# Kernel optimization log

Hardware: AMD Instinct MI355X
Metric: run time of the kernel (lower is better)

The kernel has to match this reference:

```python
import jax, jax.numpy as jnp
import numpy as np
from jax import lax

INPUT_DIM = 1024
HIDDEN_DIM = 2048
N, L = 64, 512


def setup_inputs() -> dict:
    key = jax.random.key(0)
    ks = jax.random.split(key, 6)
    X = jax.random.normal(ks[0], (N, L, INPUT_DIM), dtype=jnp.float32)
    H0 = jnp.zeros((N, HIDDEN_DIM), dtype=jnp.float32)
    # G-invariant layer params (DeepSets invariant map): out = w * sum(x) + b, one per gate (i,f,g,o)
    inv_scale = 1.0 / np.sqrt(INPUT_DIM)
    inv_w = jax.random.normal(ks[1], (4, HIDDEN_DIM), dtype=jnp.float32) * inv_scale
    inv_b = jax.random.normal(ks[2], (4, HIDDEN_DIM), dtype=jnp.float32) * inv_scale
    # Linear(hidden, hidden) per gate, torch convention W: (out, in)
    lin_scale = 1.0 / np.sqrt(HIDDEN_DIM)
    lin_W = jax.random.normal(ks[3], (4, HIDDEN_DIM, HIDDEN_DIM), dtype=jnp.float32) * lin_scale
    lin_b = jax.random.normal(ks[4], (4, HIDDEN_DIM), dtype=jnp.float32) * lin_scale
    return {"X": X, "H0": H0, "inv_w": inv_w, "inv_b": inv_b, "lin_W": lin_W, "lin_b": lin_b}


def reference(X, H0, inv_w, inv_b, lin_W, lin_b):
    # X: (N, L, D); H0: (N, H)
    def step(carry, x_t):
        h, c = carry                               # (N, H), (N, H)
        s = jnp.sum(x_t, axis=-1, keepdims=True)   # (N, 1) invariant statistic
        inv = s * inv_w[:, None, :] + inv_b[:, None, :]            # (4, N, H)
        lin = jnp.einsum('nh,gkh->gnk', h, lin_W) + lin_b[:, None, :]  # (4, N, H)
        z = inv + lin
        i = jax.nn.sigmoid(z[0])
        f = jax.nn.sigmoid(z[1])
        g = jnp.tanh(z[2])
        o = jax.nn.sigmoid(z[3])
        c = f * c + i * g
        h = o * jnp.tanh(c)
        return (h, c), None

    Xt = jnp.swapaxes(X, 0, 1)                     # (L, N, D)
    (h, _), _ = lax.scan(step, (H0, jnp.zeros_like(H0)), Xt)
    # original returns swapdims(hidden_state, 0, 1) -> (H, N)
    return h.T
```

## Files before the change

kernel.cpp:

```cpp
#include <hip/hip_runtime.h>
#include <hip/hip_fp16.h>


typedef _Float16 f16x8 __attribute__((ext_vector_type(8)));
typedef float    f32x4 __attribute__((ext_vector_type(4)));
typedef unsigned long long u64;

static __device__ __forceinline__ float fast_sig(float x) {
  return 1.f / (1.f + __expf(-x));
}
static __device__ __forceinline__ float fast_tanh(float x) {
  x = fminf(15.f, fmaxf(-15.f, x));
  const float e = __expf(2.f * x);
  return (e - 1.f) / (e + 1.f);
}

static __device__ __forceinline__ void st_h16(void* p, float v) {
  const unsigned short b = __builtin_bit_cast(unsigned short, (_Float16)v);
  __hip_atomic_store((unsigned short*)p, b, __ATOMIC_RELAXED, __HIP_MEMORY_SCOPE_AGENT);
}
static __device__ __forceinline__ void st_h64(void* p, u64 v) {
  __hip_atomic_store((u64*)p, v, __ATOMIC_RELAXED, __HIP_MEMORY_SCOPE_AGENT);
}

static __device__ __forceinline__ int h_off(int n, int j) {
  return ((n >> 4) << 16) + ((j >> 5) << 10) + ((n & 15) << 6) +
         (((j >> 3) & 3) << 4) + ((j & 7) << 1);
}

__global__ void __launch_bounds__(256) seq_sum_kernel(const float* __restrict__ X,
                                                      float* s_all) {
  const int gw   = (int)((blockIdx.x * blockDim.x + threadIdx.x) >> 6);
  const int lane = threadIdx.x & 63;
  const int n = gw >> 9, t = gw & 511;
  const float4* p = (const float4*)(X + ((size_t)gw << 10));
  float s = 0.f;
#pragma unroll
  for (int i = 0; i < 4; ++i) {
    const float4 v = p[lane + (i << 6)];
    s += (v.x + v.y) + (v.z + v.w);
  }
#pragma unroll
  for (int off = 32; off; off >>= 1) s += __shfl_xor(s, off);
  if (lane == 0) s_all[(t << 6) + n] = s;
}

__global__ void bar_init_kernel(unsigned* bar) {
  bar[threadIdx.x]       = 0u;
  bar[threadIdx.x + 256] = 0u;
  bar[threadIdx.x + 512] = 0u;
  bar[threadIdx.x + 768] = 0u;
}

static __device__ __forceinline__ void grid_barrier2(unsigned* bar, unsigned round,
                                                     int tid, int blk) {
  asm volatile("s_waitcnt vmcnt(0)" ::: "memory");
  __syncthreads();
  if (tid == 0) {
    unsigned* grp  = bar + ((blk & 7) << 5);
    unsigned* root = bar + 512;
    const unsigned old =
        __hip_atomic_fetch_add(grp, 1u, __ATOMIC_RELAXED, __HIP_MEMORY_SCOPE_AGENT);
    if (old == 32u * round - 1u)
      __hip_atomic_fetch_add(root, 1u, __ATOMIC_RELAXED, __HIP_MEMORY_SCOPE_AGENT);
    const unsigned target = 8u * round;
    unsigned guard = 0;
    while (__hip_atomic_load(root, __ATOMIC_RELAXED, __HIP_MEMORY_SCOPE_AGENT) <
           target) {
      __builtin_amdgcn_s_sleep(1);
      if (++guard > (1u << 23)) break;
    }
  }
  __syncthreads();
}

#define LOAD4(d0, d1, d2, d3, addr)                                         \
  asm volatile("global_load_dwordx4 %0, %4, off sc1\n\t"                    \
               "global_load_dwordx4 %1, %4, off offset:1024 sc1\n\t"        \
               "global_load_dwordx4 %2, %4, off offset:2048 sc1\n\t"        \
               "global_load_dwordx4 %3, %4, off offset:3072 sc1"            \
               : "=&v"(d0), "=&v"(d1), "=&v"(d2), "=&v"(d3)                 \
               : "v"(addr)                                                  \
               : "memory")

#define WAITG(n, A)                                                         \
  asm volatile("s_waitcnt vmcnt(" #n ")"                                    \
               : "+v"(A[0]), "+v"(A[1]), "+v"(A[2]), "+v"(A[3]),            \
                 "+v"(A[4]), "+v"(A[5]), "+v"(A[6]), "+v"(A[7]),            \
                 "+v"(A[8]), "+v"(A[9]), "+v"(A[10]), "+v"(A[11]),          \
                 "+v"(A[12]), "+v"(A[13]), "+v"(A[14]), "+v"(A[15])         \
               :                                                            \
               : "memory")

#define KMATH(A)                                                            \
  _Pragma("unroll")                                                         \
  for (int i_ = 0; i_ < 16; ++i_) {                                         \
    acc[0] = __builtin_amdgcn_mfma_f32_16x16x32_f16(A[i_], Wr[i_][0],       \
                                                    acc[0], 0, 0, 0);       \
    acc[1] = __builtin_amdgcn_mfma_f32_16x16x32_f16(A[i_], Wr[i_][1],       \
                                                    acc[1], 0, 0, 0);       \
    acc[2] = __builtin_amdgcn_mfma_f32_16x16x32_f16(A[i_], Wr[i_][2],       \
                                                    acc[2], 0, 0, 0);       \
    acc[3] = __builtin_amdgcn_mfma_f32_16x16x32_f16(A[i_], Wr[i_][3],       \
                                                    acc[3], 0, 0, 0);       \
  }

#define SCATTER(bt)                                                         \
  _Pragma("unroll")                                                         \
  for (int ct_ = 0; ct_ < 4; ++ct_) {                                       \
    const int kf_ = ct_ * 4 + (cc >> 2);                                    \
    _Pragma("unroll")                                                       \
    for (int v_ = 0; v_ < 4; ++v_) {                                        \
      const int n_  = (bt) * 16 + (q << 2) + v_;                            \
      const int key = (n_ & 15) ^ (n_ >> 4);                                \
      red[wave][n_][((kf_ ^ key) << 2) + (cc & 3)] = acc[ct_][v_];          \
    }                                                                       \
  }

__global__ void __launch_bounds__(256, 1) ginv_lstm_persist(
    const float* __restrict__ lin_W, const float* __restrict__ inv_w,
    const float* __restrict__ inv_b, const float* __restrict__ lin_b,
    const float* s_all, const float* __restrict__ H0,
    _Float16* hb0, _Float16* hb1, unsigned* bar, float* out) {
  __shared__ __align__(16) float red[12][32][64];
  __shared__ __align__(16) _Float16 hx[32][16];
  const int blk = blockIdx.x;
  const int tid = threadIdx.x;
  _Float16* hbuf[2] = {hb0, hb1};

  const int fblk = blk & 127;
  const int nh   = blk >> 7;

  const int wave = tid >> 6;
  const int lane = tid & 63;
  const int q    = lane >> 4;
  const int cc   = lane & 15;

  f16x8 Wr[16][4];
#pragma unroll
  for (int ct = 0; ct < 4; ++ct) {
    const int kf = ct * 4 + (cc >> 2), g = cc & 3;
    const float* wrow =
        lin_W + (((size_t)(g * 2048 + fblk * 16 + kf)) << 11) + wave * 512 + q * 8;
#pragma unroll
    for (int kc = 0; kc < 16; ++kc) {
      const float4 va = *(const float4*)(wrow + kc * 32);
      const float4 vb = *(const float4*)(wrow + kc * 32 + 4);
      f16x8 f;
      f[0] = (_Float16)va.x; f[1] = (_Float16)va.y;
      f[2] = (_Float16)va.z; f[3] = (_Float16)va.w;
      f[4] = (_Float16)vb.x; f[5] = (_Float16)vb.y;
      f[6] = (_Float16)vb.z; f[7] = (_Float16)vb.w;
      Wr[kc][ct] = f;
    }
  }

  {
    int i0 = blk * 512 + tid;
    st_h16((char*)hb0 + h_off(i0 >> 11, i0 & 2047), H0[i0]);
    i0 += 256;
    st_h16((char*)hb0 + h_off(i0 >> 11, i0 & 2047), H0[i0]);
  }

  const int nloc = lane & 31;
  const int nb   = lane >> 5;
  float iw[2][4], ibb[2][4];
#pragma unroll
  for (int kk = 0; kk < 2; ++kk) {
    const int kf = wave + (nb << 2) + (kk << 3);
    const int Kg = fblk * 16 + kf;
#pragma unroll
    for (int g = 0; g < 4; ++g) {
      iw[kk][g]  = inv_w[(g << 11) + Kg];
      ibb[kk][g] = inv_b[(g << 11) + Kg] + lin_b[(g << 11) + Kg];
    }
  }

  unsigned round = 1;
  grid_barrier2(bar, round, tid, blk);

  float cst[2] = {0.f, 0.f};

  const int ld_base = ((nh * 2) << 16) + (wave << 14) + (cc << 6) + (q << 4);
  const int st_off = ((nh * 2 + (tid >> 4)) << 16) + ((fblk >> 1) << 10) +
                     ((tid & 15) << 6) + ((fblk & 1) << 5);

  for (int t = 0; t < 512; ++t) {
    const char* hpb = (const char*)hbuf[t & 1] + ld_base;

    const float sv = s_all[(t << 6) + nh * 32 + nloc];

    f16x8 pa[16], pb[16];
    f32x4 acc[4];

#pragma unroll
    for (int w = 0; w < 4; ++w)
      LOAD4(pa[w * 4], pa[w * 4 + 1], pa[w * 4 + 2], pa[w * 4 + 3],
            hpb + (w << 12));
#pragma unroll
    for (int w = 0; w < 4; ++w)
      LOAD4(pb[w * 4], pb[w * 4 + 1], pb[w * 4 + 2], pb[w * 4 + 3],
            hpb + 65536 + (w << 12));

    WAITG(16, pa);
#pragma unroll
    for (int ct = 0; ct < 4; ++ct) acc[ct] = (f32x4){0.f, 0.f, 0.f, 0.f};
    KMATH(pa);
    SCATTER(0);

    WAITG(0, pb);
#pragma unroll
    for (int ct = 0; ct < 4; ++ct) acc[ct] = (f32x4){0.f, 0.f, 0.f, 0.f};
    KMATH(pb);
    SCATTER(1);

    __syncthreads();

    float hnew[2];
    const int key = (nloc & 15) ^ (nloc >> 4);
#pragma unroll
    for (int kk = 0; kk < 2; ++kk) {
      const int kf  = wave + (nb << 2) + (kk << 3);
      const int off = (kf ^ key) << 2;
      f32x4 zz = *(const f32x4*)&red[0][nloc][off];
#pragma unroll
      for (int w = 1; w < 4; ++w) zz += *(const f32x4*)&red[w][nloc][off];
      const float zi = zz[0] + sv * iw[kk][0] + ibb[kk][0];
      const float zf = zz[1] + sv * iw[kk][1] + ibb[kk][1];
      const float zg = zz[2] + sv * iw[kk][2] + ibb[kk][2];
      const float zo = zz[3] + sv * iw[kk][3] + ibb[kk][3];
      const float ig = fast_sig(zi);
      const float fg = fast_sig(zf);
      const float gg = fast_tanh(zg);
      const float og = fast_sig(zo);
      const float cn = fg * cst[kk] + ig * gg;
      cst[kk] = cn;
      hnew[kk] = og * fast_tanh(cn);
    }

#pragma unroll
    for (int kk = 0; kk < 2; ++kk)
      hx[nloc][wave + (nb << 2) + (kk << 3)] = (_Float16)hnew[kk];
    __syncthreads();
    if (t < 511 && tid < 32) {
      union { f16x8 v; u64 w[2]; } u0, u1;
      u0.v = *(const f16x8*)&hx[tid][0];
      u1.v = *(const f16x8*)&hx[tid][8];
      char* dst = (char*)hbuf[(t + 1) & 1] + st_off;
      st_h64(dst,      u0.w[0]);
      st_h64(dst + 8,  u0.w[1]);
      st_h64(dst + 16, u1.w[0]);
      st_h64(dst + 24, u1.w[1]);
    }
    ++round;
    grid_barrier2(bar, round, tid, blk);
  }

  if (tid < 32) {
#pragma unroll
    for (int f = 0; f < 16; ++f)
      out[((fblk * 16 + f) << 6) + nh * 32 + tid] = (float)hx[tid][f];
  }
}

extern "C" void kernel_launch(void* const* d_in, const int* in_sizes, int n_in,
                              void* d_out, int out_size, void* d_ws, size_t ws_size,
                              hipStream_t stream) {
  const float* X     = (const float*)d_in[0];
  const float* H0    = (const float*)d_in[1];
  const float* inv_w = (const float*)d_in[2];
  const float* inv_b = (const float*)d_in[3];
  const float* lin_W = (const float*)d_in[4];
  const float* lin_b = (const float*)d_in[5];
  float* out = (float*)d_out;

  const size_t S_BYTES = 512 * 64 * 4;
  const size_t BAR_PAD = 4096;
  const size_t H_BYTES = 64 * 2048 * 2;
  const size_t NEED = S_BYTES + BAR_PAD + 2 * H_BYTES;

  float*    s_all;
  unsigned* bar;
  _Float16* hb[2];
  if (ws_size >= NEED) {
    char* ws = (char*)d_ws;
    s_all = (float*)ws;
    bar   = (unsigned*)(ws + S_BYTES);
    for (int i = 0; i < 2; ++i)
      hb[i] = (_Float16*)(ws + S_BYTES + BAR_PAD + (size_t)i * H_BYTES);
  } else {
    s_all = (float*)d_out;
    char* xt = (char*)d_in[0] + (size_t)64 * 512 * 1024 * 4 -
               (BAR_PAD + 2 * H_BYTES);
    bar = (unsigned*)xt;
    for (int i = 0; i < 2; ++i)
      hb[i] = (_Float16*)(xt + BAR_PAD + (size_t)i * H_BYTES);
  }

  seq_sum_kernel<<<8192, 256, 0, stream>>>(X, s_all);
  bar_init_kernel<<<1, 256, 0, stream>>>(bar);
  ginv_lstm_persist<<<256, 256, 0, stream>>>(lin_W, inv_w, inv_b, lin_b, s_all, H0,
                                             hb[0], hb[1], bar, out);
}
```

Before: 4.079 ms.

## Flatten grid barrier, store h directly per thread, preload sequence sums into LDS

```diff
diff --git a/kernel.cpp b/kernel.cpp
--- a/kernel.cpp
+++ b/kernel.cpp
@@ -19,8 +19,8 @@
   const unsigned short b = __builtin_bit_cast(unsigned short, (_Float16)v);
   __hip_atomic_store((unsigned short*)p, b, __ATOMIC_RELAXED, __HIP_MEMORY_SCOPE_AGENT);
 }
-static __device__ __forceinline__ void st_h64(void* p, u64 v) {
-  __hip_atomic_store((u64*)p, v, __ATOMIC_RELAXED, __HIP_MEMORY_SCOPE_AGENT);
+static __device__ __forceinline__ void st_h32(void* p, unsigned v) {
+  __hip_atomic_store((unsigned*)p, v, __ATOMIC_RELAXED, __HIP_MEMORY_SCOPE_AGENT);
 }
 
 static __device__ __forceinline__ int h_off(int n, int j) {
@@ -52,21 +52,22 @@
   bar[threadIdx.x + 768] = 0u;
 }
 
-static __device__ __forceinline__ void grid_barrier2(unsigned* bar, unsigned round,
-                                                     int tid, int blk) {
+static __device__ __forceinline__ void grid_barrier(unsigned* bar, unsigned round,
+                                                    int tid, int blk) {
   asm volatile("s_waitcnt vmcnt(0)" ::: "memory");
   __syncthreads();
   if (tid == 0) {
-    unsigned* grp  = bar + ((blk & 7) << 5);
-    unsigned* root = bar + 512;
-    const unsigned old =
-        __hip_atomic_fetch_add(grp, 1u, __ATOMIC_RELAXED, __HIP_MEMORY_SCOPE_AGENT);
-    if (old == 32u * round - 1u)
-      __hip_atomic_fetch_add(root, 1u, __ATOMIC_RELAXED, __HIP_MEMORY_SCOPE_AGENT);
-    const unsigned target = 8u * round;
+    __hip_atomic_fetch_add(bar + ((blk & 7) << 4), 1u, __ATOMIC_RELAXED,
+                           __HIP_MEMORY_SCOPE_AGENT);
+    const unsigned target = round << 8;
     unsigned guard = 0;
-    while (__hip_atomic_load(root, __ATOMIC_RELAXED, __HIP_MEMORY_SCOPE_AGENT) <
-           target) {
+    for (;;) {
+      unsigned s = 0;
+#pragma unroll
+      for (int i = 0; i < 8; ++i)
+        s += __hip_atomic_load(bar + (i << 4), __ATOMIC_RELAXED,
+                               __HIP_MEMORY_SCOPE_AGENT);
+      if (s >= target) break;
       __builtin_amdgcn_s_sleep(1);
       if (++guard > (1u << 23)) break;
     }
@@ -122,8 +123,8 @@
     const float* __restrict__ inv_b, const float* __restrict__ lin_b,
     const float* s_all, const float* __restrict__ H0,
     _Float16* hb0, _Float16* hb1, unsigned* bar, float* out) {
-  __shared__ __align__(16) float red[12][32][64];
-  __shared__ __align__(16) _Float16 hx[32][16];
+  __shared__ __align__(16) float s_lds[512][32];
+  __shared__ __align__(16) float red[4][32][64];
   const int blk = blockIdx.x;
   const int tid = threadIdx.x;
   _Float16* hbuf[2] = {hb0, hb1};
@@ -162,13 +163,18 @@
     st_h16((char*)hb0 + h_off(i0 >> 11, i0 & 2047), H0[i0]);
   }
 
-  const int nloc = lane & 31;
-  const int nb   = lane >> 5;
+  for (int i = tid; i < 512 * 8; i += 256) {
+    const int t4 = i >> 3, nl4 = (i & 7) << 2;
+    *(float4*)&s_lds[t4][nl4] =
+        *(const float4*)&s_all[(t4 << 6) + (nh << 5) + nl4];
+  }
+
+  const int nloc = (wave << 3) + (lane >> 3);
+  const int c0   = (lane & 7) << 1;
   float iw[2][4], ibb[2][4];
 #pragma unroll
   for (int kk = 0; kk < 2; ++kk) {
-    const int kf = wave + (nb << 2) + (kk << 3);
-    const int Kg = fblk * 16 + kf;
+    const int Kg = fblk * 16 + c0 + kk;
 #pragma unroll
     for (int g = 0; g < 4; ++g) {
       iw[kk][g]  = inv_w[(g << 11) + Kg];
@@ -177,18 +183,18 @@
   }
 
   unsigned round = 1;
-  grid_barrier2(bar, round, tid, blk);
+  grid_barrier(bar, round, tid, blk);
 
   float cst[2] = {0.f, 0.f};
+  float hnew[2] = {0.f, 0.f};
 
   const int ld_base = ((nh * 2) << 16) + (wave << 14) + (cc << 6) + (q << 4);
-  const int st_off = ((nh * 2 + (tid >> 4)) << 16) + ((fblk >> 1) << 10) +
-                     ((tid & 15) << 6) + ((fblk & 1) << 5);
+  const int hst_off = ((nh * 2 + (nloc >> 4)) << 16) + ((fblk >> 1) << 10) +
+                      ((nloc & 15) << 6) + ((fblk & 1) << 5) + (c0 << 1);
+  const int key = (nloc & 15) ^ (nloc >> 4);
 
   for (int t = 0; t < 512; ++t) {
     const char* hpb = (const char*)hbuf[t & 1] + ld_base;
-
-    const float sv = s_all[(t << 6) + nh * 32 + nloc];
 
     f16x8 pa[16], pb[16];
     f32x4 acc[4];
@@ -216,12 +222,10 @@
 
     __syncthreads();
 
-    float hnew[2];
-    const int key = (nloc & 15) ^ (nloc >> 4);
+    const float sv = s_lds[t][nloc];
 #pragma unroll
     for (int kk = 0; kk < 2; ++kk) {
-      const int kf  = wave + (nb << 2) + (kk << 3);
-      const int off = (kf ^ key) << 2;
+      const int off = ((c0 + kk) ^ key) << 2;
       f32x4 zz = *(const f32x4*)&red[0][nloc][off];
 #pragma unroll
       for (int w = 1; w < 4; ++w) zz += *(const f32x4*)&red[w][nloc][off];
@@ -238,29 +242,18 @@
       hnew[kk] = og * fast_tanh(cn);
     }
 
-#pragma unroll
-    for (int kk = 0; kk < 2; ++kk)
-      hx[nloc][wave + (nb << 2) + (kk << 3)] = (_Float16)hnew[kk];
-    __syncthreads();
-    if (t < 511 && tid < 32) {
-      union { f16x8 v; u64 w[2]; } u0, u1;
-      u0.v = *(const f16x8*)&hx[tid][0];
-      u1.v = *(const f16x8*)&hx[tid][8];
-      char* dst = (char*)hbuf[(t + 1) & 1] + st_off;
-      st_h64(dst,      u0.w[0]);
-      st_h64(dst + 8,  u0.w[1]);
-      st_h64(dst + 16, u1.w[0]);
-      st_h64(dst + 24, u1.w[1]);
+    {
+      const unsigned lo = __builtin_bit_cast(unsigned short, (_Float16)hnew[0]);
+      const unsigned hi = __builtin_bit_cast(unsigned short, (_Float16)hnew[1]);
+      st_h32((char*)hbuf[(t + 1) & 1] + hst_off, lo | (hi << 16));
     }
     ++round;
-    grid_barrier2(bar, round, tid, blk);
-  }
-
-  if (tid < 32) {
-#pragma unroll
-    for (int f = 0; f < 16; ++f)
-      out[((fblk * 16 + f) << 6) + nh * 32 + tid] = (float)hx[tid][f];
-  }
+    grid_barrier(bar, round, tid, blk);
+  }
+
+#pragma unroll
+  for (int kk = 0; kk < 2; ++kk)
+    out[((fblk * 16 + c0 + kk) << 6) + (nh << 5) + nloc] = hnew[kk];
 }
 
 extern "C" void kernel_launch(void* const* d_in, const int* in_sizes, int n_in,
```

After: 4.194 ms. 1.03x slower.
